# Optimization experiments

Hardware: AMD Instinct MI355X
Metric: run time of the kernel (lower is better)

Reference implementation:

```python
import jax, jax.numpy as jnp
import numpy as np

E = 1_000_000   # number of multicut edges
T = 2_000_000   # number of triplets (GNN nodes)
M = 4_000_000   # number of directed GNN edges among triplets
HID = 32


def gcn_conv(x, edge_index, W, b, n):
    """PyG GCNConv: x' = D^-1/2 (A+I) D^-1/2 (x W) + b, symmetric norm with self-loops."""
    src, dst = edge_index[0], edge_index[1]
    xw = x @ W                                        # [n, out]
    deg = jnp.zeros((n,), xw.dtype).at[dst].add(1.0) + 1.0  # +1 self-loop
    dis = jax.lax.rsqrt(deg)                          # deg^-1/2
    norm = dis[src] * dis[dst]                        # [M]
    msg = xw[src] * norm[:, None]                     # gather + scale
    out = jax.ops.segment_sum(msg, dst, num_segments=n)
    out = out + xw * (dis * dis)[:, None]             # self-loop contribution
    return out + b


def setup_inputs() -> dict:
    key = jax.random.key(0)
    ks = jax.random.split(key, 16)
    inp = {
        "edge_costs": jax.random.normal(ks[0], (E,), jnp.float32),
        "t12": jax.random.normal(ks[1], (T,), jnp.float32),
        "t13": jax.random.normal(ks[2], (T,), jnp.float32),
        "t23": jax.random.normal(ks[3], (T,), jnp.float32),
        "corr_12": jax.random.randint(ks[4], (T,), 0, E),
        "corr_13": jax.random.randint(ks[5], (T,), 0, E),
        "corr_23": jax.random.randint(ks[6], (T,), 0, E),
        # counts >= 1 so the divide is well-defined (as in real triplet decompositions)
        "edge_counter": jax.random.randint(ks[7], (E,), 1, 6).astype(jnp.float32),
        "edge_index": jax.random.randint(ks[8], (2, M), 0, T),
        # GCNConv / Linear parameters (glorot-ish scale)
        "W1": jax.random.normal(ks[9], (3, HID), jnp.float32) * (1.0 / np.sqrt(3)),
        "b1": jnp.zeros((HID,), jnp.float32),
        "W2": jax.random.normal(ks[10], (HID, HID), jnp.float32) * (1.0 / np.sqrt(HID)),
        "b2": jnp.zeros((HID,), jnp.float32),
        "Wout": jax.random.normal(ks[11], (HID, 3), jnp.float32) * (1.0 / np.sqrt(HID)),
        "bout": jnp.zeros((3,), jnp.float32),
    }
    return inp


def reference(edge_costs, t12, t13, t23, corr_12, corr_13, corr_23,
              edge_counter, edge_index, W1, b1, W2, b2, Wout, bout):
    # --- send_messages_to_triplets: gather / divide, then zero covered edges ---
    t12 = t12 + edge_costs[corr_12] / edge_counter[corr_12]
    t13 = t13 + edge_costs[corr_13] / edge_counter[corr_13]
    t23 = t23 + edge_costs[corr_23] / edge_counter[corr_23]
    edge_costs = jnp.where(edge_counter > 0, jnp.zeros_like(edge_costs), edge_costs)

    # --- send_messages_to_edges: 2-layer GCN over triplet nodes + linear head ---
    tri = jnp.stack([t12, t13, t23], axis=1)          # [T, 3]
    x = jax.nn.relu(gcn_conv(tri, edge_index, W1, b1, T))
    x = jax.nn.relu(gcn_conv(x, edge_index, W2, b2, T))
    delta = x @ Wout + bout                           # [T, 3]

    t12 = t12 - delta[:, 0]
    t13 = t13 - delta[:, 1]
    t23 = t23 - delta[:, 2]

    edge_updates = (jnp.zeros_like(edge_costs)
                    .at[corr_12].add(delta[:, 0])
                    .at[corr_13].add(delta[:, 1])
                    .at[corr_23].add(delta[:, 2]))
    edge_costs = edge_costs + edge_updates
    return (edge_costs, t12, t13, t23)
```

## Files before the change

kernel.cpp:

```cpp
#include <hip/hip_runtime.h>
#include <hip/hip_fp16.h>
#include <math.h>

#define HID 32
#define BS 256

#define NPB 2048
#define NBK_MAX 1024
#define EBT 8192
#define CAP 6912

#define NPB_E 2048

typedef _Float16 h2v __attribute__((ext_vector_type(2)));

__device__ __forceinline__ h2v u2h(uint u) { return __builtin_bit_cast(h2v, u); }
__device__ __forceinline__ uint h2u(h2v h) { return __builtin_bit_cast(uint, h); }
__device__ __forceinline__ uint pack2(float a, float b) {
  h2v r; r.x = (_Float16)a; r.y = (_Float16)b; return h2u(r);
}
__device__ __forceinline__ float dot2acc(uint a, uint b, float c) {
#if __has_builtin(__builtin_amdgcn_fdot2)
  return __builtin_amdgcn_fdot2(u2h(a), u2h(b), c, false);
#else
  h2v ah = u2h(a), bh = u2h(b);
  c = fmaf((float)ah.x, (float)bh.x, c);
  return fmaf((float)ah.y, (float)bh.y, c);
#endif
}
__device__ __forceinline__ float h4w(uint2 g) {
  h2v hi = u2h(g.y); return (float)hi.y;
}


__global__ __launch_bounds__(BS) void k_bhist2(const int* __restrict__ ei,
                                               int* __restrict__ thist, int M, int NBK) {
  __shared__ int hist[NBK_MAX];
  for (int b = threadIdx.x; b < NBK; b += BS) hist[b] = 0;
  __syncthreads();
  int e0 = blockIdx.x * EBT;
  int n = min(EBT, M - e0);
  for (int k = threadIdx.x; k < n; k += BS) {
    int d = ei[M + e0 + k];
    atomicAdd(&hist[d / NPB], 1);
  }
  __syncthreads();
  for (int b = threadIdx.x; b < NBK; b += BS)
    thist[blockIdx.x * NBK + b] = hist[b];
}

__global__ __launch_bounds__(BS) void k_ehist2(const int* __restrict__ c12,
                                               const int* __restrict__ c13,
                                               const int* __restrict__ c23,
                                               int* __restrict__ thist, int T, int NBK) {
  __shared__ int hist[NBK_MAX];
  for (int b = threadIdx.x; b < NBK; b += BS) hist[b] = 0;
  __syncthreads();
  int N3 = 3 * T;
  int j0 = blockIdx.x * EBT;
  int n = min(EBT, N3 - j0);
  for (int k = threadIdx.x; k < n; k += BS) {
    int j = j0 + k;
    int key = (j < T) ? c12[j] : ((j < 2 * T) ? c13[j - T] : c23[j - 2 * T]);
    atomicAdd(&hist[key / NPB_E], 1);
  }
  __syncthreads();
  for (int b = threadIdx.x; b < NBK; b += BS)
    thist[blockIdx.x * NBK + b] = hist[b];
}

__global__ __launch_bounds__(BS) void k_tbase(const int* __restrict__ thist,
                                              int* __restrict__ tbase,
                                              int* __restrict__ gh, int NBK, int NT) {
  __shared__ int part[BS];
  int b = blockIdx.x;
  int C = (NT + BS - 1) / BS;
  int s = 0;
  for (int k = 0; k < C; ++k) {
    int t = threadIdx.x * C + k;
    if (t < NT) s += thist[t * NBK + b];
  }
  part[threadIdx.x] = s;
  __syncthreads();
  for (int off = 1; off < BS; off <<= 1) {
    int v = part[threadIdx.x];
    int u = (threadIdx.x >= off) ? part[threadIdx.x - off] : 0;
    __syncthreads();
    part[threadIdx.x] = v + u;
    __syncthreads();
  }
  int run = (threadIdx.x > 0) ? part[threadIdx.x - 1] : 0;
  for (int k = 0; k < C; ++k) {
    int t = threadIdx.x * C + k;
    if (t < NT) {
      int v = thist[t * NBK + b];
      tbase[t * NBK + b] = run;
      run += v;
    }
  }
  if (threadIdx.x == BS - 1) gh[b] = run;
}

__global__ __launch_bounds__(BS) void k_bscan(const int* __restrict__ gh,
                                              int* __restrict__ gboff,
                                              int* __restrict__ gcur, int NBK) {
  __shared__ int part[BS];
  int C = (NBK + BS - 1) / BS;
  int s = 0;
  for (int k = 0; k < C; ++k) {
    int idx = threadIdx.x * C + k;
    if (idx < NBK) s += gh[idx];
  }
  part[threadIdx.x] = s;
  __syncthreads();
  for (int off = 1; off < BS; off <<= 1) {
    int v = part[threadIdx.x];
    int u = (threadIdx.x >= off) ? part[threadIdx.x - off] : 0;
    __syncthreads();
    part[threadIdx.x] = v + u;
    __syncthreads();
  }
  int run = (threadIdx.x > 0) ? part[threadIdx.x - 1] : 0;
  for (int k = 0; k < C; ++k) {
    int idx = threadIdx.x * C + k;
    if (idx < NBK) {
      gboff[idx] = run;
      gcur[idx] = run;
      run += gh[idx];
    }
  }
  if (threadIdx.x == BS - 1) gboff[NBK] = run;
}

__global__ __launch_bounds__(BS) void k_bplace(const int* __restrict__ ei,
                                               const int* __restrict__ gboff,
                                               const int* __restrict__ tbase,
                                               uint* __restrict__ P, int M, int NBK) {
  __shared__ int cur[NBK_MAX];
  int t = blockIdx.x;
  for (int b = threadIdx.x; b < NBK; b += BS)
    cur[b] = gboff[b] + tbase[t * NBK + b];
  __syncthreads();
  int e0 = t * EBT;
  int n = min(EBT, M - e0);
  for (int k = threadIdx.x; k < n; k += BS) {
    uint sidx = (uint)ei[e0 + k];
    int d = ei[M + e0 + k];
    int pos = atomicAdd(&cur[d / NPB], 1);
    P[pos] = ((uint)(d & (NPB - 1)) << 21) | sidx;
  }
}

__global__ __launch_bounds__(BS) void k_escatv(const int* __restrict__ c12,
                                               const int* __restrict__ c13,
                                               const int* __restrict__ c23,
                                               const float* __restrict__ dd,
                                               const int* __restrict__ gboff,
                                               const int* __restrict__ tbase,
                                               int2* __restrict__ PEV, int T, int NBK) {
  __shared__ int cur[NBK_MAX];
  int t = blockIdx.x;
  for (int b = threadIdx.x; b < NBK; b += BS)
    cur[b] = gboff[b] + tbase[t * NBK + b];
  __syncthreads();
  int N3 = 3 * T;
  int j0 = t * EBT;
  int n = min(EBT, N3 - j0);
  for (int k = threadIdx.x; k < n; k += BS) {
    int j = j0 + k;
    int key = (j < T) ? c12[j] : ((j < 2 * T) ? c13[j - T] : c23[j - 2 * T]);
    float v = dd[j];
    int pos = atomicAdd(&cur[key / NPB_E], 1);
    PEV[pos] = make_int2(key, __builtin_bit_cast(int, v));
  }
}


__global__ __launch_bounds__(BS) void k_bfinal(const uint* __restrict__ P,
                                               const int* __restrict__ gboff,
                                               int* __restrict__ row_ptr,
                                               int* __restrict__ srt, int T, int M,
                                               int NBK) {
  __shared__ int cnt[NPB];
  __shared__ int lsrt[CAP];
  __shared__ int part[BS];
  int b = blockIdx.x;
  int d0 = b * NPB;
  int nodesHere = min(NPB, T - d0);
  int p0 = gboff[b], p1 = gboff[b + 1];
  int nE = p1 - p0;
  for (int j = threadIdx.x; j < NPB; j += BS) cnt[j] = 0;
  __syncthreads();
  for (int j = threadIdx.x; j < nE; j += BS) {
    uint p = P[p0 + j];
    atomicAdd(&cnt[p >> 21], 1);
  }
  __syncthreads();
  const int CN = NPB / BS;
  int s = 0;
#pragma unroll
  for (int k = 0; k < CN; ++k) s += cnt[threadIdx.x * CN + k];
  part[threadIdx.x] = s;
  __syncthreads();
  for (int off = 1; off < BS; off <<= 1) {
    int v = part[threadIdx.x];
    int u = (threadIdx.x >= off) ? part[threadIdx.x - off] : 0;
    __syncthreads();
    part[threadIdx.x] = v + u;
    __syncthreads();
  }
  int run = (threadIdx.x > 0) ? part[threadIdx.x - 1] : 0;
#pragma unroll
  for (int k = 0; k < CN; ++k) {
    int idx = threadIdx.x * CN + k;
    int c = cnt[idx];
    cnt[idx] = run;
    if (idx < nodesHere) row_ptr[d0 + idx] = p0 + run;
    run += c;
  }
  if (b == NBK - 1 && threadIdx.x == 0) row_ptr[T] = M;
  __syncthreads();
  if (nE <= CAP) {
    for (int j = threadIdx.x; j < nE; j += BS) {
      uint p = P[p0 + j];
      int pos = atomicAdd(&cnt[p >> 21], 1);
      lsrt[pos] = (int)(p & 0x1FFFFFu);
    }
    __syncthreads();
    for (int j = threadIdx.x; j < nE; j += BS) srt[p0 + j] = lsrt[j];
  } else {
    for (int j = threadIdx.x; j < nE; j += BS) {
      uint p = P[p0 + j];
      int pos = atomicAdd(&cnt[p >> 21], 1);
      srt[p0 + pos] = (int)(p & 0x1FFFFFu);
    }
  }
}

__global__ __launch_bounds__(BS) void k_oecsum2(const int2* __restrict__ PEV,
                                                const int* __restrict__ gboff,
                                                float* __restrict__ oec, int E) {
  __shared__ float acc[NPB_E];
  int b = blockIdx.x;
  int e0 = b * NPB_E;
  int p0 = gboff[b], p1 = gboff[b + 1];
  int n = p1 - p0;
  for (int j = threadIdx.x; j < NPB_E; j += BS) acc[j] = 0.0f;
  __syncthreads();
  int k = threadIdx.x;
  for (; k + 3 * BS < n; k += 4 * BS) {
    int2 q0 = PEV[p0 + k];
    int2 q1 = PEV[p0 + k + BS];
    int2 q2 = PEV[p0 + k + 2 * BS];
    int2 q3 = PEV[p0 + k + 3 * BS];
    atomicAdd(&acc[q0.x - e0], __builtin_bit_cast(float, q0.y));
    atomicAdd(&acc[q1.x - e0], __builtin_bit_cast(float, q1.y));
    atomicAdd(&acc[q2.x - e0], __builtin_bit_cast(float, q2.y));
    atomicAdd(&acc[q3.x - e0], __builtin_bit_cast(float, q3.y));
  }
  for (; k < n; k += BS) {
    int2 q = PEV[p0 + k];
    atomicAdd(&acc[q.x - e0], __builtin_bit_cast(float, q.y));
  }
  __syncthreads();
  int lim = min(NPB_E, E - e0);
  for (int j = threadIdx.x; j < lim; j += BS) oec[e0 + j] += acc[j];
}


__global__ void k_prep_e(const float* __restrict__ ec, const float* __restrict__ cnt,
                         float* __restrict__ msg, float* __restrict__ oec, int E) {
  int i = blockIdx.x * BS + threadIdx.x;
  if (i >= E) return;
  float c = cnt[i], v = ec[i];
  msg[i] = v / c;
  oec[i] = (c > 0.0f) ? 0.0f : v;
}

__global__ void k_step1pack(const float* __restrict__ msg,
                            const float* __restrict__ t12, const float* __restrict__ t13,
                            const float* __restrict__ t23,
                            const int* __restrict__ c12, const int* __restrict__ c13,
                            const int* __restrict__ c23,
                            const int* __restrict__ row_ptr,
                            uint2* __restrict__ trih, int T) {
  int i = blockIdx.x * BS + threadIdx.x;
  if (i >= T) return;
  int a = c12[i], b = c13[i], c = c23[i];
  float vx = t12[i] + msg[a];
  float vy = t13[i] + msg[b];
  float vz = t23[i] + msg[c];
  float vw = rsqrtf((float)(row_ptr[i + 1] - row_ptr[i]) + 1.0f);
  uint2 h;
  h.x = pack2(vx, vy);
  h.y = pack2(vz, vw);
  trih[i] = h;
}

__global__ void k_packw(const float* __restrict__ W1, const float* __restrict__ b1,
                        const float* __restrict__ W2, uint* __restrict__ pkw) {
  int i = blockIdx.x * BS + threadIdx.x;
  if (i < 48) {
    int r = i >> 4, k = i & 15;
    pkw[i] = pack2(W1[r * HID + 2 * k], W1[r * HID + 2 * k + 1]);
  } else if (i < 64) {
    int k = i - 48;
    pkw[i] = pack2(b1[2 * k], b1[2 * k + 1]);
  } else if (i < 576) {
    int idx = i - 64;
    int h2 = idx >> 5, j = idx & 31;
    pkw[i] = pack2(W2[(2 * h2) * HID + j], W2[(2 * h2 + 1) * HID + j]);
  }
}

__device__ __forceinline__ void acc3(uint2 g, float di, float& ax, float& ay, float& az) {
  h2v lo = u2h(g.x), hi = u2h(g.y);
  float w = (float)hi.y * di;
  ax = fmaf((float)lo.x, w, ax);
  ay = fmaf((float)lo.y, w, ay);
  az = fmaf((float)hi.x, w, az);
}

__global__ __launch_bounds__(BS) void k_agg1c(const int* __restrict__ row_ptr,
                                              const int* __restrict__ srt,
                                              const uint2* __restrict__ trih,
                                              uint2* __restrict__ G4h, int T) {
  int i = blockIdx.x * BS + threadIdx.x;
  if (i >= T) return;
  int r0 = row_ptr[i], r1 = row_ptr[i + 1];
  uint2 ts = trih[i];
  h2v tlo = u2h(ts.x), thi = u2h(ts.y);
  float di = (float)thi.y;
  float d2 = di * di;
  float ax = (float)tlo.x * d2, ay = (float)tlo.y * d2, az = (float)thi.x * d2;
  int e = r0;
  for (; e + 4 <= r1; e += 4) {
    int s0 = srt[e + 0];
    int s1 = srt[e + 1];
    int s2 = srt[e + 2];
    int s3 = srt[e + 3];
    uint2 g0 = trih[s0];
    uint2 g1 = trih[s1];
    uint2 g2 = trih[s2];
    uint2 g3 = trih[s3];
    acc3(g0, di, ax, ay, az);
    acc3(g1, di, ax, ay, az);
    acc3(g2, di, ax, ay, az);
    acc3(g3, di, ax, ay, az);
  }
  for (; e < r1; ++e) {
    uint2 g = trih[srt[e]];
    acc3(g, di, ax, ay, az);
  }
  uint2 o;
  o.x = pack2(ax, ay);
  o.y = pack2(az, di);
  G4h[i] = o;
}

__device__ __forceinline__ void edge_h1_accu(uint2 g, float w,
                                             const uint* __restrict__ W1s,
                                             const uint* __restrict__ b1s,
                                             float* S) {
  h2v lo = u2h(g.x), hi = u2h(g.y);
  h2v hx; hx.x = lo.x; hx.y = lo.x;
  h2v hy; hy.x = lo.y; hy.y = lo.y;
  h2v hz; hz.x = hi.x; hz.y = hi.x;
  h2v zero; zero.x = (_Float16)0.f; zero.y = (_Float16)0.f;
#pragma unroll
  for (int k = 0; k < 16; ++k) {
    h2v t = hx * u2h(W1s[k]) + (hy * u2h(W1s[16 + k]) + (hz * u2h(W1s[32 + k]) + u2h(b1s[k])));
    t = __builtin_elementwise_max(t, zero);
    S[2 * k]     = fmaf((float)t.x, w, S[2 * k]);
    S[2 * k + 1] = fmaf((float)t.y, w, S[2 * k + 1]);
  }
}

__global__ __launch_bounds__(BS) void k_l2head(
    const int* __restrict__ row_ptr, const int* __restrict__ srt,
    const uint2* __restrict__ G4h, const uint2* __restrict__ trih,
    const uint* __restrict__ pkw,
    const float* __restrict__ b2,
    const float* __restrict__ Wout, const float* __restrict__ bout,
    float* __restrict__ o12, float* __restrict__ o13, float* __restrict__ o23,
    float* __restrict__ dd, int T) {
  int i = blockIdx.x * BS + threadIdx.x;
  if (i >= T) return;
  int r0 = row_ptr[i], r1 = row_ptr[i + 1];
  uint2 gs = G4h[i];
  uint2 tp = trih[i];
  h2v tlo = u2h(tp.x), thi = u2h(tp.y);
  float di = (float)thi.y;
  const uint* W1s = pkw;
  const uint* b1s = pkw + 48;
  const uint* W2s = pkw + 64;

  float S[HID];
#pragma unroll
  for (int h = 0; h < HID; ++h) S[h] = 0.0f;

  edge_h1_accu(gs, di * di, W1s, b1s, S);

  int e = r0;
  for (; e + 4 <= r1; e += 4) {
    int s0 = srt[e + 0];
    int s1 = srt[e + 1];
    int s2 = srt[e + 2];
    int s3 = srt[e + 3];
    uint2 g0 = G4h[s0];
    uint2 g1 = G4h[s1];
    uint2 g2 = G4h[s2];
    uint2 g3 = G4h[s3];
    float w0 = h4w(g0) * di;
    float w1 = h4w(g1) * di;
    float w2 = h4w(g2) * di;
    float w3 = h4w(g3) * di;
    edge_h1_accu(g0, w0, W1s, b1s, S);
    edge_h1_accu(g1, w1, W1s, b1s, S);
    edge_h1_accu(g2, w2, W1s, b1s, S);
    edge_h1_accu(g3, w3, W1s, b1s, S);
  }
  if (e + 2 <= r1) {
    int s0 = srt[e + 0];
    int s1 = srt[e + 1];
    uint2 g0 = G4h[s0];
    uint2 g1 = G4h[s1];
    float w0 = h4w(g0) * di;
    float w1 = h4w(g1) * di;
    edge_h1_accu(g0, w0, W1s, b1s, S);
    edge_h1_accu(g1, w1, W1s, b1s, S);
    e += 2;
  }
  if (e < r1) {
    uint2 g = G4h[srt[e]];
    edge_h1_accu(g, h4w(g) * di, W1s, b1s, S);
  }

  uint sh[16];
#pragma unroll
  for (int k = 0; k < 16; ++k) sh[k] = pack2(S[2 * k], S[2 * k + 1]);

  float d0 = bout[0], d1 = bout[1], dd2 = bout[2];
#pragma unroll
  for (int cz = 0; cz < 4; ++cz) {
    float z[8];
#pragma unroll
    for (int j = 0; j < 8; ++j) z[j] = b2[cz * 8 + j];
#pragma unroll
    for (int h2 = 0; h2 < 16; ++h2) {
#pragma unroll
      for (int j = 0; j < 8; ++j)
        z[j] = dot2acc(sh[h2], W2s[h2 * HID + cz * 8 + j], z[j]);
    }
#pragma unroll
    for (int j = 0; j < 8; ++j) {
      float v = fmaxf(z[j], 0.0f);
      int jp = cz * 8 + j;
      d0  = fmaf(v, Wout[jp * 3 + 0], d0);
      d1  = fmaf(v, Wout[jp * 3 + 1], d1);
      dd2 = fmaf(v, Wout[jp * 3 + 2], dd2);
    }
  }

  o12[i] = (float)tlo.x - d0;
  o13[i] = (float)tlo.y - d1;
  o23[i] = (float)thi.x - dd2;
  dd[i] = d0;
  dd[T + i] = d1;
  dd[2 * T + i] = dd2;
}


extern "C" void kernel_launch(void* const* d_in, const int* in_sizes, int n_in,
                              void* d_out, int out_size, void* d_ws, size_t ws_size,
                              hipStream_t stream) {
  const float* ec  = (const float*)d_in[0];
  const float* t12 = (const float*)d_in[1];
  const float* t13 = (const float*)d_in[2];
  const float* t23 = (const float*)d_in[3];
  const int* c12   = (const int*)d_in[4];
  const int* c13   = (const int*)d_in[5];
  const int* c23   = (const int*)d_in[6];
  const float* cnt = (const float*)d_in[7];
  const int* ei    = (const int*)d_in[8];
  const float* W1  = (const float*)d_in[9];
  const float* b1  = (const float*)d_in[10];
  const float* W2  = (const float*)d_in[11];
  const float* b2  = (const float*)d_in[12];
  const float* Wout = (const float*)d_in[13];
  const float* bout = (const float*)d_in[14];

  const int E = in_sizes[0];
  const int T = in_sizes[1];
  const int M = in_sizes[8] / 2;
  const int NBK = (T + NPB - 1) / NPB;
  const int NBK_E = (E + NPB_E - 1) / NPB_E;

  float* oec = (float*)d_out;
  float* o12 = oec + E;
  float* o13 = o12 + T;
  float* o23 = o13 + T;

  auto blocks = [](long n) { return (int)((n + BS - 1) / BS); };
  const int tiles   = (M + EBT - 1) / EBT;
  const int tiles_e = (3 * T + EBT - 1) / EBT;

  uint2*  trih = (uint2*)d_ws;
  uint2*  G4h  = trih + T;
  int2*   PEV  = (int2*)(G4h + T);
  float*  dd   = (float*)(PEV + 3 * (size_t)T);
  int*    srt  = (int*)(dd + 3 * (size_t)T);
  int*    rptr = srt + M;
  float*  msg  = (float*)(rptr + (T + 1));
  int*    gh   = (int*)(msg + E);
  int*    gboff = gh + NBK;
  int*    gcur  = gboff + (NBK + 1);
  uint*   pkw   = (uint*)(gcur + NBK);
  int*    gh_e  = (int*)(pkw + 576);
  int*    gboff_e = gh_e + NBK_E;
  int*    gcur_e  = gboff_e + (NBK_E + 1);
  int*    thist_n = gcur_e + NBK_E;
  int*    tbase_n = thist_n + (size_t)tiles * NBK;
  int*    thist_e = tbase_n + (size_t)tiles * NBK;
  int*    tbase_e = thist_e + (size_t)tiles_e * NBK_E;
  uint*   P    = (uint*)PEV;

  k_bhist2<<<tiles, BS, 0, stream>>>(ei, thist_n, M, NBK);
  k_tbase<<<NBK, BS, 0, stream>>>(thist_n, tbase_n, gh, NBK, tiles);
  k_bscan<<<1, BS, 0, stream>>>(gh, gboff, gcur, NBK);
  k_bplace<<<tiles, BS, 0, stream>>>(ei, gboff, tbase_n, P, M, NBK);
  k_bfinal<<<NBK, BS, 0, stream>>>(P, gboff, rptr, srt, T, M, NBK);

  k_ehist2<<<tiles_e, BS, 0, stream>>>(c12, c13, c23, thist_e, T, NBK_E);
  k_tbase<<<NBK_E, BS, 0, stream>>>(thist_e, tbase_e, gh_e, NBK_E, tiles_e);
  k_bscan<<<1, BS, 0, stream>>>(gh_e, gboff_e, gcur_e, NBK_E);

  k_packw<<<3, BS, 0, stream>>>(W1, b1, W2, pkw);
  k_prep_e<<<blocks(E), BS, 0, stream>>>(ec, cnt, msg, oec, E);
  k_step1pack<<<blocks(T), BS, 0, stream>>>(msg, t12, t13, t23, c12, c13, c23,
                                            rptr, trih, T);

  k_agg1c<<<blocks(T), BS, 0, stream>>>(rptr, srt, trih, G4h, T);

  k_l2head<<<blocks(T), BS, 0, stream>>>(rptr, srt, G4h, trih, pkw,
                                         b2, Wout, bout,
                                         o12, o13, o23, dd, T);

  k_escatv<<<tiles_e, BS, 0, stream>>>(c12, c13, c23, dd, gboff_e, tbase_e,
                                       PEV, T, NBK_E);
  k_oecsum2<<<NBK_E, BS, 0, stream>>>(PEV, gboff_e, oec, E);
}
```

Baseline: 594.8 us.

## Merge histogram, scan and prep kernels to cut launches and edge-array passes

Combines the node and edge histogram kernels plus weight packing into one launch, merges the two tbase and two bscan launches, and drops the gcur outputs. The separate edge prep pass is removed: the message divide moves into the triplet pack kernel and the edge-cost zeroing moves into the final scatter-sum. EBT doubles, halving the number of tiles and the per-tile histogram rows. This removes several launches and a full E-sized read/write pass, at the cost of extra gathers of counts in the pack kernel and less parallelism in the histogram and place kernels.

```diff
diff --git a/kernel.cpp b/kernel.cpp
--- a/kernel.cpp
+++ b/kernel.cpp
@@ -7,7 +7,7 @@
 
 #define NPB 2048
 #define NBK_MAX 1024
-#define EBT 8192
+#define EBT 16384
 #define CAP 6912
 
 #define NPB_E 2048
@@ -33,47 +33,67 @@
 }
 
 
-__global__ __launch_bounds__(BS) void k_bhist2(const int* __restrict__ ei,
-                                               int* __restrict__ thist, int M, int NBK) {
+__global__ __launch_bounds__(BS) void k_hist_all(
+    const int* __restrict__ ei, const int* __restrict__ c12,
+    const int* __restrict__ c13, const int* __restrict__ c23,
+    const float* __restrict__ W1, const float* __restrict__ b1,
+    const float* __restrict__ W2,
+    int* __restrict__ thist_n, int* __restrict__ thist_e, uint* __restrict__ pkw,
+    int M, int T, int NBK_N, int NBK_E, int TIL_N, int TIL_E) {
   __shared__ int hist[NBK_MAX];
-  for (int b = threadIdx.x; b < NBK; b += BS) hist[b] = 0;
-  __syncthreads();
-  int e0 = blockIdx.x * EBT;
-  int n = min(EBT, M - e0);
-  for (int k = threadIdx.x; k < n; k += BS) {
-    int d = ei[M + e0 + k];
-    atomicAdd(&hist[d / NPB], 1);
-  }
-  __syncthreads();
-  for (int b = threadIdx.x; b < NBK; b += BS)
-    thist[blockIdx.x * NBK + b] = hist[b];
-}
-
-__global__ __launch_bounds__(BS) void k_ehist2(const int* __restrict__ c12,
-                                               const int* __restrict__ c13,
-                                               const int* __restrict__ c23,
-                                               int* __restrict__ thist, int T, int NBK) {
-  __shared__ int hist[NBK_MAX];
-  for (int b = threadIdx.x; b < NBK; b += BS) hist[b] = 0;
-  __syncthreads();
-  int N3 = 3 * T;
-  int j0 = blockIdx.x * EBT;
-  int n = min(EBT, N3 - j0);
-  for (int k = threadIdx.x; k < n; k += BS) {
-    int j = j0 + k;
-    int key = (j < T) ? c12[j] : ((j < 2 * T) ? c13[j - T] : c23[j - 2 * T]);
-    atomicAdd(&hist[key / NPB_E], 1);
-  }
-  __syncthreads();
-  for (int b = threadIdx.x; b < NBK; b += BS)
-    thist[blockIdx.x * NBK + b] = hist[b];
-}
-
-__global__ __launch_bounds__(BS) void k_tbase(const int* __restrict__ thist,
-                                              int* __restrict__ tbase,
-                                              int* __restrict__ gh, int NBK, int NT) {
+  int bid = blockIdx.x;
+  if (bid < TIL_N) {
+    for (int b = threadIdx.x; b < NBK_N; b += BS) hist[b] = 0;
+    __syncthreads();
+    int e0 = bid * EBT;
+    int n = min(EBT, M - e0);
+    for (int k = threadIdx.x; k < n; k += BS) {
+      int d = ei[M + e0 + k];
+      atomicAdd(&hist[d / NPB], 1);
+    }
+    __syncthreads();
+    for (int b = threadIdx.x; b < NBK_N; b += BS)
+      thist_n[bid * NBK_N + b] = hist[b];
+  } else if (bid < TIL_N + TIL_E) {
+    int t = bid - TIL_N;
+    for (int b = threadIdx.x; b < NBK_E; b += BS) hist[b] = 0;
+    __syncthreads();
+    int N3 = 3 * T;
+    int j0 = t * EBT;
+    int n = min(EBT, N3 - j0);
+    for (int k = threadIdx.x; k < n; k += BS) {
+      int j = j0 + k;
+      int key = (j < T) ? c12[j] : ((j < 2 * T) ? c13[j - T] : c23[j - 2 * T]);
+      atomicAdd(&hist[key / NPB_E], 1);
+    }
+    __syncthreads();
+    for (int b = threadIdx.x; b < NBK_E; b += BS)
+      thist_e[t * NBK_E + b] = hist[b];
+  } else {
+    int i = (bid - TIL_N - TIL_E) * BS + threadIdx.x;
+    if (i < 48) {
+      int r = i >> 4, k = i & 15;
+      pkw[i] = pack2(W1[r * HID + 2 * k], W1[r * HID + 2 * k + 1]);
+    } else if (i < 64) {
+      int k = i - 48;
+      pkw[i] = pack2(b1[2 * k], b1[2 * k + 1]);
+    } else if (i < 576) {
+      int idx = i - 64;
+      int h2 = idx >> 5, j = idx & 31;
+      pkw[i] = pack2(W2[(2 * h2) * HID + j], W2[(2 * h2 + 1) * HID + j]);
+    }
+  }
+}
+
+__global__ __launch_bounds__(BS) void k_tbase_all(
+    const int* __restrict__ thist_n, int* __restrict__ tbase_n, int* __restrict__ gh_n,
+    const int* __restrict__ thist_e, int* __restrict__ tbase_e, int* __restrict__ gh_e,
+    int NBK_N, int NT_N, int NBK_E, int NT_E) {
   __shared__ int part[BS];
-  int b = blockIdx.x;
+  int bid = blockIdx.x;
+  const int* thist; int* tbase; int* gh; int b; int NT; int NBK;
+  if (bid < NBK_N) { thist = thist_n; tbase = tbase_n; gh = gh_n; b = bid; NT = NT_N; NBK = NBK_N; }
+  else             { thist = thist_e; tbase = tbase_e; gh = gh_e; b = bid - NBK_N; NT = NT_E; NBK = NBK_E; }
   int C = (NT + BS - 1) / BS;
   int s = 0;
   for (int k = 0; k < C; ++k) {
@@ -101,10 +121,13 @@
   if (threadIdx.x == BS - 1) gh[b] = run;
 }
 
-__global__ __launch_bounds__(BS) void k_bscan(const int* __restrict__ gh,
-                                              int* __restrict__ gboff,
-                                              int* __restrict__ gcur, int NBK) {
+__global__ __launch_bounds__(BS) void k_bscan2(
+    const int* __restrict__ gh_n, int* __restrict__ gboff_n, int NBK_N,
+    const int* __restrict__ gh_e, int* __restrict__ gboff_e, int NBK_E) {
   __shared__ int part[BS];
+  const int* gh; int* gboff; int NBK;
+  if (blockIdx.x == 0) { gh = gh_n; gboff = gboff_n; NBK = NBK_N; }
+  else                 { gh = gh_e; gboff = gboff_e; NBK = NBK_E; }
   int C = (NBK + BS - 1) / BS;
   int s = 0;
   for (int k = 0; k < C; ++k) {
@@ -125,7 +148,6 @@
     int idx = threadIdx.x * C + k;
     if (idx < NBK) {
       gboff[idx] = run;
-      gcur[idx] = run;
       run += gh[idx];
     }
   }
@@ -237,9 +259,11 @@
   }
 }
 
-__global__ __launch_bounds__(BS) void k_oecsum2(const int2* __restrict__ PEV,
-                                                const int* __restrict__ gboff,
-                                                float* __restrict__ oec, int E) {
+__global__ __launch_bounds__(BS) void k_oecsum(const int2* __restrict__ PEV,
+                                               const int* __restrict__ gboff,
+                                               const float* __restrict__ ec,
+                                               const float* __restrict__ cnt_a,
+                                               float* __restrict__ oec, int E) {
   __shared__ float acc[NPB_E];
   int b = blockIdx.x;
   int e0 = b * NPB_E;
@@ -264,20 +288,15 @@
   }
   __syncthreads();
   int lim = min(NPB_E, E - e0);
-  for (int j = threadIdx.x; j < lim; j += BS) oec[e0 + j] += acc[j];
-}
-
-
-__global__ void k_prep_e(const float* __restrict__ ec, const float* __restrict__ cnt,
-                         float* __restrict__ msg, float* __restrict__ oec, int E) {
-  int i = blockIdx.x * BS + threadIdx.x;
-  if (i >= E) return;
-  float c = cnt[i], v = ec[i];
-  msg[i] = v / c;
-  oec[i] = (c > 0.0f) ? 0.0f : v;
-}
-
-__global__ void k_step1pack(const float* __restrict__ msg,
+  for (int j = threadIdx.x; j < lim; j += BS) {
+    int e = e0 + j;
+    float base = (cnt_a[e] > 0.0f) ? 0.0f : ec[e];
+    oec[e] = base + acc[j];
+  }
+}
+
+
+__global__ void k_step1pack(const float* __restrict__ ec, const float* __restrict__ cnt_a,
                             const float* __restrict__ t12, const float* __restrict__ t13,
                             const float* __restrict__ t23,
                             const int* __restrict__ c12, const int* __restrict__ c13,
@@ -287,30 +306,14 @@
   int i = blockIdx.x * BS + threadIdx.x;
   if (i >= T) return;
   int a = c12[i], b = c13[i], c = c23[i];
-  float vx = t12[i] + msg[a];
-  float vy = t13[i] + msg[b];
-  float vz = t23[i] + msg[c];
+  float vx = t12[i] + ec[a] / cnt_a[a];
+  float vy = t13[i] + ec[b] / cnt_a[b];
+  float vz = t23[i] + ec[c] / cnt_a[c];
   float vw = rsqrtf((float)(row_ptr[i + 1] - row_ptr[i]) + 1.0f);
   uint2 h;
   h.x = pack2(vx, vy);
   h.y = pack2(vz, vw);
   trih[i] = h;
-}
-
-__global__ void k_packw(const float* __restrict__ W1, const float* __restrict__ b1,
-                        const float* __restrict__ W2, uint* __restrict__ pkw) {
-  int i = blockIdx.x * BS + threadIdx.x;
-  if (i < 48) {
-    int r = i >> 4, k = i & 15;
-    pkw[i] = pack2(W1[r * HID + 2 * k], W1[r * HID + 2 * k + 1]);
-  } else if (i < 64) {
-    int k = i - 48;
-    pkw[i] = pack2(b1[2 * k], b1[2 * k + 1]);
-  } else if (i < 576) {
-    int idx = i - 64;
-    int h2 = idx >> 5, j = idx & 31;
-    pkw[i] = pack2(W2[(2 * h2) * HID + j], W2[(2 * h2 + 1) * HID + j]);
-  }
 }
 
 __device__ __forceinline__ void acc3(uint2 g, float di, float& ax, float& ay, float& az) {
@@ -511,33 +514,28 @@
   float*  dd   = (float*)(PEV + 3 * (size_t)T);
   int*    srt  = (int*)(dd + 3 * (size_t)T);
   int*    rptr = srt + M;
-  float*  msg  = (float*)(rptr + (T + 1));
-  int*    gh   = (int*)(msg + E);
+  int*    gh   = rptr + (T + 1);
   int*    gboff = gh + NBK;
-  int*    gcur  = gboff + (NBK + 1);
-  uint*   pkw   = (uint*)(gcur + NBK);
+  uint*   pkw   = (uint*)(gboff + (NBK + 1));
   int*    gh_e  = (int*)(pkw + 576);
   int*    gboff_e = gh_e + NBK_E;
-  int*    gcur_e  = gboff_e + (NBK_E + 1);
-  int*    thist_n = gcur_e + NBK_E;
+  int*    thist_n = gboff_e + (NBK_E + 1);
   int*    tbase_n = thist_n + (size_t)tiles * NBK;
   int*    thist_e = tbase_n + (size_t)tiles * NBK;
   int*    tbase_e = thist_e + (size_t)tiles_e * NBK_E;
   uint*   P    = (uint*)PEV;
 
-  k_bhist2<<<tiles, BS, 0, stream>>>(ei, thist_n, M, NBK);
-  k_tbase<<<NBK, BS, 0, stream>>>(thist_n, tbase_n, gh, NBK, tiles);
-  k_bscan<<<1, BS, 0, stream>>>(gh, gboff, gcur, NBK);
+  k_hist_all<<<tiles + tiles_e + 3, BS, 0, stream>>>(
+      ei, c12, c13, c23, W1, b1, W2, thist_n, thist_e, pkw,
+      M, T, NBK, NBK_E, tiles, tiles_e);
+  k_tbase_all<<<NBK + NBK_E, BS, 0, stream>>>(
+      thist_n, tbase_n, gh, thist_e, tbase_e, gh_e, NBK, tiles, NBK_E, tiles_e);
+  k_bscan2<<<2, BS, 0, stream>>>(gh, gboff, NBK, gh_e, gboff_e, NBK_E);
+
   k_bplace<<<tiles, BS, 0, stream>>>(ei, gboff, tbase_n, P, M, NBK);
   k_bfinal<<<NBK, BS, 0, stream>>>(P, gboff, rptr, srt, T, M, NBK);
 
-  k_ehist2<<<tiles_e, BS, 0, stream>>>(c12, c13, c23, thist_e, T, NBK_E);
-  k_tbase<<<NBK_E, BS, 0, stream>>>(thist_e, tbase_e, gh_e, NBK_E, tiles_e);
-  k_bscan<<<1, BS, 0, stream>>>(gh_e, gboff_e, gcur_e, NBK_E);
-
-  k_packw<<<3, BS, 0, stream>>>(W1, b1, W2, pkw);
-  k_prep_e<<<blocks(E), BS, 0, stream>>>(ec, cnt, msg, oec, E);
-  k_step1pack<<<blocks(T), BS, 0, stream>>>(msg, t12, t13, t23, c12, c13, c23,
+  k_step1pack<<<blocks(T), BS, 0, stream>>>(ec, cnt, t12, t13, t23, c12, c13, c23,
                                             rptr, trih, T);
 
   k_agg1c<<<blocks(T), BS, 0, stream>>>(rptr, srt, trih, G4h, T);
@@ -548,5 +546,5 @@
 
   k_escatv<<<tiles_e, BS, 0, stream>>>(c12, c13, c23, dd, gboff_e, tbase_e,
                                        PEV, T, NBK_E);
-  k_oecsum2<<<NBK_E, BS, 0, stream>>>(PEV, gboff_e, oec, E);
-}
+  k_oecsum<<<NBK_E, BS, 0, stream>>>(PEV, gboff_e, ec, cnt, oec, E);
+}
```

New measurement: 633.1 us. 1.06x slower.
